# Kernel optimization log

Hardware: AMD Instinct MI355X
Metric: run time of the kernel (lower is better)

The kernel has to match this reference:

```python
import jax, jax.numpy as jnp
import numpy as np


def setup_inputs() -> dict:
    key = jax.random.key(0)
    k1, k2 = jax.random.split(key)
    B, M, N, D = 8, 2048, 2048, 1024
    x = jax.random.normal(k1, (B, M, D), dtype=jnp.float32)
    y = jax.random.normal(k2, (B, N, D), dtype=jnp.float32)
    return {"x": x, "y": y}


def reference(x, y):
    # scores e[b,m,n] = <x[b,m], y[b,n]>   (K.batch_dot(x, y, axes=2))
    e = jnp.einsum('bmd,bnd->bmn', x, y)
    # stable softmax over last axis (the exp/max/sum sequence in the original)
    p = jax.nn.softmax(e, axis=-1)
    # K.batch_dot(z, x, axes=1): contract axis 1 (m) of both -> [B, n, d]; V = x
    out = jnp.einsum('bmn,bmd->bnd', p, x)
    return out
```

## Files before the change

kernel.cpp:

```cpp
#include <hip/hip_runtime.h>
#include <hip/hip_bf16.h>
#include <stdint.h>

#define B_ 8
#define M_ 2048
#define N_ 2048
#define D_ 1024

typedef __bf16 bf16x8 __attribute__((ext_vector_type(8)));
typedef float f32x4 __attribute__((ext_vector_type(4)));
typedef uint16_t us4 __attribute__((ext_vector_type(4)));
typedef uint16_t us8 __attribute__((ext_vector_type(8)));

__device__ __forceinline__ uint16_t f2b(float f) {
    uint32_t u = __float_as_uint(f);
    return (uint16_t)((u + 0x7FFFu + ((u >> 16) & 1u)) >> 16);
}
__device__ __forceinline__ float b2f(uint16_t h) {
    return __uint_as_float(((uint32_t)h) << 16);
}

__device__ __forceinline__ void gld16(const uint16_t* g, const uint16_t* l) {
    __builtin_amdgcn_global_load_lds(
        (const __attribute__((address_space(1))) uint32_t*)g,
        (__attribute__((address_space(3))) uint32_t*)l,
        16, 0, 0);
}

__global__ __launch_bounds__(256) void k_split(const float* __restrict__ x,
                                               const float* __restrict__ y,
                                               uint16_t* __restrict__ xh, uint16_t* __restrict__ xl,
                                               uint16_t* __restrict__ yh, uint16_t* __restrict__ yl) {
    const int i = (blockIdx.x * 256 + threadIdx.x) * 4;
    float4 vx = *(const float4*)(x + i);
    float4 vy = *(const float4*)(y + i);
    float fx[4] = {vx.x, vx.y, vx.z, vx.w};
    float fy[4] = {vy.x, vy.y, vy.z, vy.w};
    us4 hx, lx, hy, ly;
#pragma unroll
    for (int k = 0; k < 4; ++k) {
        uint16_t h = f2b(fx[k]);
        hx[k] = h; lx[k] = f2b(fx[k] - b2f(h));
        uint16_t g = f2b(fy[k]);
        hy[k] = g; ly[k] = f2b(fy[k] - b2f(g));
    }
    *(us4*)(xh + i) = hx;
    *(us4*)(xl + i) = lx;
    *(us4*)(yh + i) = hy;
    *(us4*)(yl + i) = ly;
}

__global__ __launch_bounds__(256) void k_gemm1(const uint16_t* __restrict__ xh,
                                               const uint16_t* __restrict__ xl,
                                               const uint16_t* __restrict__ yh,
                                               const uint16_t* __restrict__ yl,
                                               float* __restrict__ e) {
    const int b = blockIdx.z;
    const int m0 = blockIdx.x * 128;
    const int n0 = blockIdx.y * 128;
    __shared__ __align__(16) uint16_t lds[16384];

    const int tid = threadIdx.x;
    const int lane = tid & 63;
    const int wid = tid >> 6;
    const int wm = (wid & 1) * 64;
    const int wn = (wid >> 1) * 64;
    const int quad = lane >> 4;
    const int r16 = lane & 15;
    const int swz = quad ^ ((r16 >> 1) & 3);

    const uint16_t* src[4];
    src[0] = xh + ((size_t)b * M_ + m0) * D_;
    src[1] = xl + ((size_t)b * M_ + m0) * D_;
    src[2] = yh + ((size_t)b * N_ + n0) * D_;
    src[3] = yl + ((size_t)b * N_ + n0) * D_;

    f32x4 acc[4][4];
#pragma unroll
    for (int i = 0; i < 4; ++i)
#pragma unroll
        for (int j = 0; j < 4; ++j) acc[i][j] = (f32x4){0.f, 0.f, 0.f, 0.f};

    for (int kt = 0; kt < D_ / 32; ++kt) {
#pragma unroll
        for (int c = 0; c < 8; ++c) {
            const int offbase = c * 2048 + wid * 512;
            const int tile = offbase >> 12;
            const int o = (offbase & 4095) + lane * 8;
            const int row = o >> 5;
            const int gp = (o & 31) >> 3;
            const int gd = gp ^ ((row >> 1) & 3);
            gld16(src[tile] + (size_t)row * D_ + kt * 32 + gd * 8, &lds[offbase]);
        }
        __syncthreads();

        bf16x8 ah[4], al[4], bh[4], bl[4];
#pragma unroll
        for (int i = 0; i < 4; ++i) {
            const int ra = (wm + i * 16 + r16) * 32 + swz * 8;
            ah[i] = *(const bf16x8*)&lds[ra];
            al[i] = *(const bf16x8*)&lds[4096 + ra];
            const int rb = (wn + i * 16 + r16) * 32 + swz * 8;
            bh[i] = *(const bf16x8*)&lds[8192 + rb];
            bl[i] = *(const bf16x8*)&lds[12288 + rb];
        }
#pragma unroll
        for (int i = 0; i < 4; ++i)
#pragma unroll
            for (int j = 0; j < 4; ++j) {
                acc[i][j] = __builtin_amdgcn_mfma_f32_16x16x32_bf16(ah[i], bh[j], acc[i][j], 0, 0, 0);
                acc[i][j] = __builtin_amdgcn_mfma_f32_16x16x32_bf16(ah[i], bl[j], acc[i][j], 0, 0, 0);
                acc[i][j] = __builtin_amdgcn_mfma_f32_16x16x32_bf16(al[i], bh[j], acc[i][j], 0, 0, 0);
            }
        __syncthreads();
    }

    float* eb = e + (size_t)b * M_ * N_;
#pragma unroll
    for (int i = 0; i < 4; ++i) {
        const int rbase = m0 + wm + i * 16 + quad * 4;
#pragma unroll
        for (int j = 0; j < 4; ++j) {
            const int col = n0 + wn + j * 16 + r16;
#pragma unroll
            for (int r = 0; r < 4; ++r)
                eb[(size_t)(rbase + r) * N_ + col] = acc[i][j][r];
        }
    }
}

__global__ __launch_bounds__(256) void k_rowstats(const float* __restrict__ e,
                                                  float* __restrict__ mx,
                                                  float* __restrict__ inv) {
    const int row = blockIdx.x;
    const float* p = e + (size_t)row * N_;
    const int t = threadIdx.x;
    float4 v0 = ((const float4*)p)[t];
    float4 v1 = ((const float4*)p)[t + 256];
    float m = fmaxf(fmaxf(fmaxf(v0.x, v0.y), fmaxf(v0.z, v0.w)),
                    fmaxf(fmaxf(v1.x, v1.y), fmaxf(v1.z, v1.w)));
#pragma unroll
    for (int s = 32; s > 0; s >>= 1) m = fmaxf(m, __shfl_xor(m, s, 64));
    __shared__ float smax[4];
    __shared__ float ssum[4];
    const int wid = t >> 6, lane = t & 63;
    if (lane == 0) smax[wid] = m;
    __syncthreads();
    m = fmaxf(fmaxf(smax[0], smax[1]), fmaxf(smax[2], smax[3]));
    float s = __expf(v0.x - m) + __expf(v0.y - m) + __expf(v0.z - m) + __expf(v0.w - m)
            + __expf(v1.x - m) + __expf(v1.y - m) + __expf(v1.z - m) + __expf(v1.w - m);
#pragma unroll
    for (int sh = 32; sh > 0; sh >>= 1) s += __shfl_xor(s, sh, 64);
    if (lane == 0) ssum[wid] = s;
    __syncthreads();
    if (t == 0) {
        mx[row] = m;
        inv[row] = 1.0f / (ssum[0] + ssum[1] + ssum[2] + ssum[3]);
    }
}

__global__ __launch_bounds__(256) void k_texp(const float* __restrict__ e,
                                              const float* __restrict__ mx,
                                              const float* __restrict__ inv,
                                              uint16_t* __restrict__ pT) {
    const int b = blockIdx.z, m0 = blockIdx.x * 64, n0 = blockIdx.y * 64;
    __shared__ float tile[64 * 65];
    const int t = threadIdx.x;
    const float* eb = e + (size_t)b * M_ * N_;
#pragma unroll
    for (int q = 0; q < 4; ++q) {
        const int row = q * 16 + (t >> 4);
        const int c4 = (t & 15) * 4;
        float4 v = *(const float4*)&eb[(size_t)(m0 + row) * N_ + n0 + c4];
        const float mv = mx[b * M_ + m0 + row];
        const float iv = inv[b * M_ + m0 + row];
        tile[row * 65 + c4 + 0] = __expf(v.x - mv) * iv;
        tile[row * 65 + c4 + 1] = __expf(v.y - mv) * iv;
        tile[row * 65 + c4 + 2] = __expf(v.z - mv) * iv;
        tile[row * 65 + c4 + 3] = __expf(v.w - mv) * iv;
    }
    __syncthreads();
    uint16_t* pb = pT + (size_t)b * N_ * M_;
#pragma unroll
    for (int q = 0; q < 2; ++q) {
        const int n = q * 32 + (t >> 3);
        const int mc = (t & 7) * 8;
        us8 o;
#pragma unroll
        for (int k = 0; k < 8; ++k) o[k] = f2b(tile[(mc + k) * 65 + n]);
        *(us8*)&pb[(size_t)(n0 + n) * M_ + m0 + mc] = o;
    }
}

__global__ __launch_bounds__(256) void k_tx(const float* __restrict__ x,
                                            uint16_t* __restrict__ xt) {
    const int b = blockIdx.z, m0 = blockIdx.x * 64, d0 = blockIdx.y * 64;
    __shared__ float tile[64 * 65];
    const int t = threadIdx.x;
    const float* xb = x + (size_t)b * M_ * D_;
#pragma unroll
    for (int q = 0; q < 4; ++q) {
        const int row = q * 16 + (t >> 4);
        const int c4 = (t & 15) * 4;
        float4 v = *(const float4*)&xb[(size_t)(m0 + row) * D_ + d0 + c4];
        tile[row * 65 + c4 + 0] = v.x;
        tile[row * 65 + c4 + 1] = v.y;
        tile[row * 65 + c4 + 2] = v.z;
        tile[row * 65 + c4 + 3] = v.w;
    }
    __syncthreads();
    uint16_t* xtb = xt + (size_t)b * D_ * M_;
#pragma unroll
    for (int q = 0; q < 2; ++q) {
        const int d = q * 32 + (t >> 3);
        const int mc = (t & 7) * 8;
        us8 o;
#pragma unroll
        for (int k = 0; k < 8; ++k) o[k] = f2b(tile[(mc + k) * 65 + d]);
        *(us8*)&xtb[(size_t)(d0 + d) * M_ + m0 + mc] = o;
    }
}

__global__ __launch_bounds__(256) void k_gemm2(const uint16_t* __restrict__ pT,
                                               const uint16_t* __restrict__ xt,
                                               float* __restrict__ out) {
    const int b = blockIdx.z;
    const int n0 = blockIdx.x * 128;
    const int d0 = blockIdx.y * 128;
    __shared__ __align__(16) uint16_t lds[16384];

    const int tid = threadIdx.x;
    const int lane = tid & 63;
    const int wid = tid >> 6;
    const int wn = (wid & 1) * 64;
    const int wd = (wid >> 1) * 64;
    const int quad = lane >> 4;
    const int r16 = lane & 15;

    const uint16_t* srcA = pT + ((size_t)b * N_ + n0) * M_;
    const uint16_t* srcB = xt + ((size_t)b * D_ + d0) * M_;

    f32x4 acc[4][4];
#pragma unroll
    for (int i = 0; i < 4; ++i)
#pragma unroll
        for (int j = 0; j < 4; ++j) acc[i][j] = (f32x4){0.f, 0.f, 0.f, 0.f};

    for (int kt = 0; kt < M_ / 64; ++kt) {
#pragma unroll
        for (int c = 0; c < 8; ++c) {
            const int offbase = c * 2048 + wid * 512;
            const int tile = offbase >> 13;
            const int o = (offbase & 8191) + lane * 8;
            const int row = o >> 6;
            const int gp = (o & 63) >> 3;
            const int gd = gp ^ (row & 7);
            const uint16_t* sp = tile ? srcB : srcA;
            gld16(sp + (size_t)row * M_ + kt * 64 + gd * 8, &lds[offbase]);
        }
        __syncthreads();

#pragma unroll
        for (int h = 0; h < 2; ++h) {
            const int p = (h * 4 + quad) ^ (r16 & 7);
            bf16x8 a[4], bb[4];
#pragma unroll
            for (int i = 0; i < 4; ++i) {
                a[i]  = *(const bf16x8*)&lds[(wn + i * 16 + r16) * 64 + p * 8];
                bb[i] = *(const bf16x8*)&lds[8192 + (wd + i * 16 + r16) * 64 + p * 8];
            }
#pragma unroll
            for (int i = 0; i < 4; ++i)
#pragma unroll
                for (int j = 0; j < 4; ++j)
                    acc[i][j] = __builtin_amdgcn_mfma_f32_16x16x32_bf16(a[i], bb[j], acc[i][j], 0, 0, 0);
        }
        __syncthreads();
    }

    float* ob = out + (size_t)b * N_ * D_;
#pragma unroll
    for (int i = 0; i < 4; ++i) {
        const int rbase = n0 + wn + i * 16 + quad * 4;
#pragma unroll
        for (int j = 0; j < 4; ++j) {
            const int col = d0 + wd + j * 16 + r16;
#pragma unroll
            for (int r = 0; r < 4; ++r)
                ob[(size_t)(rbase + r) * D_ + col] = acc[i][j][r];
        }
    }
}

extern "C" void kernel_launch(void* const* d_in, const int* in_sizes, int n_in,
                              void* d_out, int out_size, void* d_ws, size_t ws_size,
                              hipStream_t stream) {
    const float* x = (const float*)d_in[0];
    const float* y = (const float*)d_in[1];
    float* out = (float*)d_out;
    char* ws = (char*)d_ws;

    const size_t MiB = 1024 * 1024;
    int g = 8;
    while (g > 1 && (size_t)g * 32 * MiB > ws_size) g >>= 1;
    if ((size_t)g * 32 * MiB > ws_size) return;

    const size_t T = (size_t)g * M_ * D_ * 2;
    uint16_t* xh = (uint16_t*)(ws + 0 * T);
    uint16_t* xl = (uint16_t*)(ws + 1 * T);
    uint16_t* yh = (uint16_t*)(ws + 2 * T);
    uint16_t* yl = (uint16_t*)(ws + 3 * T);
    float*    e  = (float*)(ws + 4 * T);
    float*    mx = (float*)(ws);
    float*    inv = mx + (size_t)g * M_;
    uint16_t* xt = xl;
    uint16_t* pT = yh;

    for (int c0 = 0; c0 < B_; c0 += g) {
        const float* xc = x + (size_t)c0 * M_ * D_;
        const float* yc = y + (size_t)c0 * N_ * D_;
        float* oc = out + (size_t)c0 * N_ * D_;

        hipLaunchKernelGGL(k_split, dim3((g * M_ * D_) / (256 * 4)), dim3(256), 0, stream,
                           xc, yc, xh, xl, yh, yl);
        hipLaunchKernelGGL(k_gemm1, dim3(M_ / 128, N_ / 128, g), dim3(256), 0, stream,
                           xh, xl, yh, yl, e);
        hipLaunchKernelGGL(k_rowstats, dim3(g * M_), dim3(256), 0, stream, e, mx, inv);
        hipLaunchKernelGGL(k_texp, dim3(M_ / 64, N_ / 64, g), dim3(256), 0, stream,
                           e, mx, inv, pT);
        hipLaunchKernelGGL(k_tx, dim3(M_ / 64, D_ / 64, g), dim3(256), 0, stream, xc, xt);
        hipLaunchKernelGGL(k_gemm2, dim3(N_ / 128, D_ / 128, g), dim3(256), 0, stream,
                           pT, xt, oc);
    }
}
```

Measured before the change: 543.2 us.

## Enlarge GEMM1 tiles with double-buffered LDS and fuse partial softmax row stats

GEMM1 moves to 256x256 tiles with 512 threads, a double-buffered LDS pipeline that prefetches the next k-slice in two halves, and setprio/barrier scheduling around the MFMA groups. Its epilogue now computes per-64-column partial row max and exp-sums, and a small combine kernel merges them. This replaces the separate rowstats pass, which re-read the whole score matrix. The cost is 128 KiB of LDS per block and more registers, which limits occupancy. The partial stats are stored in the tail of the output buffer, which is safe only if that region is written after the last use.

Measured after the change: 507.4 us. -6.6%, faster.

```diff
diff --git a/kernel.cpp b/kernel.cpp
--- a/kernel.cpp
+++ b/kernel.cpp
@@ -50,113 +50,143 @@
     *(us4*)(yl + i) = ly;
 }
 
-__global__ __launch_bounds__(256) void k_gemm1(const uint16_t* __restrict__ xh,
-                                               const uint16_t* __restrict__ xl,
-                                               const uint16_t* __restrict__ yh,
-                                               const uint16_t* __restrict__ yl,
-                                               float* __restrict__ e) {
+__global__ __launch_bounds__(512, 2) void k_gemm1(const uint16_t* __restrict__ xh,
+                                                  const uint16_t* __restrict__ xl,
+                                                  const uint16_t* __restrict__ yh,
+                                                  const uint16_t* __restrict__ yl,
+                                                  float* __restrict__ e,
+                                                  float* __restrict__ pmax,
+                                                  float* __restrict__ psum) {
     const int b = blockIdx.z;
-    const int m0 = blockIdx.x * 128;
-    const int n0 = blockIdx.y * 128;
-    __shared__ __align__(16) uint16_t lds[16384];
+    const int m0 = blockIdx.x * 256;
+    const int n0 = blockIdx.y * 256;
+    __shared__ __align__(16) uint16_t lds[65536];
 
     const int tid = threadIdx.x;
     const int lane = tid & 63;
     const int wid = tid >> 6;
-    const int wm = (wid & 1) * 64;
-    const int wn = (wid >> 1) * 64;
+    const int wm = (wid >> 2) * 128;
+    const int wn = (wid & 3) * 64;
     const int quad = lane >> 4;
     const int r16 = lane & 15;
-    const int swz = quad ^ ((r16 >> 1) & 3);
-
-    const uint16_t* src[4];
-    src[0] = xh + ((size_t)b * M_ + m0) * D_;
-    src[1] = xl + ((size_t)b * M_ + m0) * D_;
-    src[2] = yh + ((size_t)b * N_ + n0) * D_;
-    src[3] = yl + ((size_t)b * N_ + n0) * D_;
-
-    f32x4 acc[4][4];
-#pragma unroll
-    for (int i = 0; i < 4; ++i)
+    const int swz8 = (quad ^ ((r16 >> 1) & 3)) * 8;
+
+    const int base_row = wid * 16 + (lane >> 2);
+    const int gd8 = ((lane & 3) ^ ((lane >> 3) & 3)) * 8;
+    const uint16_t* gp[4];
+    gp[0] = xh + ((size_t)b * M_ + m0 + base_row) * D_ + gd8;
+    gp[1] = xl + ((size_t)b * M_ + m0 + base_row) * D_ + gd8;
+    gp[2] = yh + ((size_t)b * N_ + n0 + base_row) * D_ + gd8;
+    gp[3] = yl + ((size_t)b * N_ + n0 + base_row) * D_ + gd8;
+    const int ldsW = wid * 512;
+
+    const int abase = (wm + r16) * 32 + swz8;
+    const int bbase = 16384 + (wn + r16) * 32 + swz8;
+
+    f32x4 acc[8][4];
+#pragma unroll
+    for (int i = 0; i < 8; ++i)
 #pragma unroll
         for (int j = 0; j < 4; ++j) acc[i][j] = (f32x4){0.f, 0.f, 0.f, 0.f};
 
+    auto STAGE = [&](int dst, int ktn, int c0, int c1) {
+#pragma unroll
+        for (int c = c0; c < c1; ++c)
+            gld16(gp[c >> 1] + (size_t)(c & 1) * (128 * D_) + ktn * 32,
+                  &lds[dst + c * 4096 + ldsW]);
+    };
+
+    STAGE(0, 0, 0, 8);
+
     for (int kt = 0; kt < D_ / 32; ++kt) {
-#pragma unroll
-        for (int c = 0; c < 8; ++c) {
-            const int offbase = c * 2048 + wid * 512;
-            const int tile = offbase >> 12;
-            const int o = (offbase & 4095) + lane * 8;
-            const int row = o >> 5;
-            const int gp = (o & 31) >> 3;
-            const int gd = gp ^ ((row >> 1) & 3);
-            gld16(src[tile] + (size_t)row * D_ + kt * 32 + gd * 8, &lds[offbase]);
-        }
-        __syncthreads();
-
-        bf16x8 ah[4], al[4], bh[4], bl[4];
-#pragma unroll
-        for (int i = 0; i < 4; ++i) {
-            const int ra = (wm + i * 16 + r16) * 32 + swz * 8;
-            ah[i] = *(const bf16x8*)&lds[ra];
-            al[i] = *(const bf16x8*)&lds[4096 + ra];
-            const int rb = (wn + i * 16 + r16) * 32 + swz * 8;
-            bh[i] = *(const bf16x8*)&lds[8192 + rb];
-            bl[i] = *(const bf16x8*)&lds[12288 + rb];
-        }
-#pragma unroll
-        for (int i = 0; i < 4; ++i)
+        const int bo = (kt & 1) << 15;
+        const int nbo = bo ^ 32768;
+
+        if (kt < D_ / 32 - 1) {
+            STAGE(nbo, kt + 1, 0, 4);
+            asm volatile("s_waitcnt vmcnt(4)" ::: "memory");
+        } else {
+            asm volatile("s_waitcnt vmcnt(0)" ::: "memory");
+        }
+        __builtin_amdgcn_s_barrier();
+        __builtin_amdgcn_sched_barrier(0);
+
+        bf16x8 bh[4], bl[4], ah[8], al[8];
+#pragma unroll
+        for (int j = 0; j < 4; ++j) {
+            bh[j] = *(const bf16x8*)&lds[bo + bbase + j * 512];
+            bl[j] = *(const bf16x8*)&lds[bo + bbase + 8192 + j * 512];
+        }
+        auto RDA = [&](int i) {
+            ah[i] = *(const bf16x8*)&lds[bo + abase + i * 512];
+            al[i] = *(const bf16x8*)&lds[bo + abase + 8192 + i * 512];
+        };
+        auto MM = [&](int i) {
 #pragma unroll
             for (int j = 0; j < 4; ++j) {
                 acc[i][j] = __builtin_amdgcn_mfma_f32_16x16x32_bf16(ah[i], bh[j], acc[i][j], 0, 0, 0);
                 acc[i][j] = __builtin_amdgcn_mfma_f32_16x16x32_bf16(ah[i], bl[j], acc[i][j], 0, 0, 0);
                 acc[i][j] = __builtin_amdgcn_mfma_f32_16x16x32_bf16(al[i], bh[j], acc[i][j], 0, 0, 0);
             }
-        __syncthreads();
+        };
+
+        RDA(0); RDA(1); RDA(2); RDA(3);
+        __builtin_amdgcn_s_setprio(1); MM(0); MM(1); __builtin_amdgcn_s_setprio(0);
+        __builtin_amdgcn_s_barrier(); __builtin_amdgcn_sched_barrier(0);
+        if (kt < D_ / 32 - 1) STAGE(nbo, kt + 1, 4, 8);
+        RDA(4); RDA(5);
+        __builtin_amdgcn_s_setprio(1); MM(2); MM(3); __builtin_amdgcn_s_setprio(0);
+        __builtin_amdgcn_s_barrier(); __builtin_amdgcn_sched_barrier(0);
+        RDA(6); RDA(7);
+        __builtin_amdgcn_s_setprio(1); MM(4); MM(5); __builtin_amdgcn_s_setprio(0);
+        __builtin_amdgcn_s_barrier(); __builtin_amdgcn_sched_barrier(0);
+        __builtin_amdgcn_s_setprio(1); MM(6); MM(7); __builtin_amdgcn_s_setprio(0);
+        __builtin_amdgcn_s_barrier(); __builtin_amdgcn_sched_barrier(0);
     }
 
     float* eb = e + (size_t)b * M_ * N_;
-#pragma unroll
-    for (int i = 0; i < 4; ++i) {
-        const int rbase = m0 + wm + i * 16 + quad * 4;
-#pragma unroll
-        for (int j = 0; j < 4; ++j) {
-            const int col = n0 + wn + j * 16 + r16;
-#pragma unroll
-            for (int r = 0; r < 4; ++r)
-                eb[(size_t)(rbase + r) * N_ + col] = acc[i][j][r];
-        }
-    }
-}
-
-__global__ __launch_bounds__(256) void k_rowstats(const float* __restrict__ e,
-                                                  float* __restrict__ mx,
-                                                  float* __restrict__ inv) {
-    const int row = blockIdx.x;
-    const float* p = e + (size_t)row * N_;
-    const int t = threadIdx.x;
-    float4 v0 = ((const float4*)p)[t];
-    float4 v1 = ((const float4*)p)[t + 256];
-    float m = fmaxf(fmaxf(fmaxf(v0.x, v0.y), fmaxf(v0.z, v0.w)),
-                    fmaxf(fmaxf(v1.x, v1.y), fmaxf(v1.z, v1.w)));
-#pragma unroll
-    for (int s = 32; s > 0; s >>= 1) m = fmaxf(m, __shfl_xor(m, s, 64));
-    __shared__ float smax[4];
-    __shared__ float ssum[4];
-    const int wid = t >> 6, lane = t & 63;
-    if (lane == 0) smax[wid] = m;
-    __syncthreads();
-    m = fmaxf(fmaxf(smax[0], smax[1]), fmaxf(smax[2], smax[3]));
-    float s = __expf(v0.x - m) + __expf(v0.y - m) + __expf(v0.z - m) + __expf(v0.w - m)
-            + __expf(v1.x - m) + __expf(v1.y - m) + __expf(v1.z - m) + __expf(v1.w - m);
-#pragma unroll
-    for (int sh = 32; sh > 0; sh >>= 1) s += __shfl_xor(s, sh, 64);
-    if (lane == 0) ssum[wid] = s;
-    __syncthreads();
-    if (t == 0) {
-        mx[row] = m;
-        inv[row] = 1.0f / (ssum[0] + ssum[1] + ssum[2] + ssum[3]);
-    }
+    const int grows = (int)gridDim.z * M_;
+    const int growbase = b * M_ + m0 + wm;
+    const int nb = (n0 + wn) >> 6;
+    float* pm = pmax + (size_t)nb * grows + growbase;
+    float* ps = psum + (size_t)nb * grows + growbase;
+
+#pragma unroll
+    for (int i = 0; i < 8; ++i) {
+#pragma unroll
+        for (int r = 0; r < 4; ++r) {
+            const float v0 = acc[i][0][r], v1 = acc[i][1][r];
+            const float v2 = acc[i][2][r], v3 = acc[i][3][r];
+            float mrow = fmaxf(fmaxf(v0, v1), fmaxf(v2, v3));
+#pragma unroll
+            for (int s = 1; s < 16; s <<= 1) mrow = fmaxf(mrow, __shfl_xor(mrow, s, 64));
+            float srow = __expf(v0 - mrow) + __expf(v1 - mrow)
+                       + __expf(v2 - mrow) + __expf(v3 - mrow);
+#pragma unroll
+            for (int s = 1; s < 16; s <<= 1) srow += __shfl_xor(srow, s, 64);
+            const int lrow = i * 16 + quad * 4 + r;
+            if (r16 == 0) { pm[lrow] = mrow; ps[lrow] = srow; }
+            const size_t ebase = (size_t)(m0 + wm + lrow) * N_ + n0 + wn + r16;
+#pragma unroll
+            for (int j = 0; j < 4; ++j) eb[ebase + j * 16] = acc[i][j][r];
+        }
+    }
+}
+
+__global__ __launch_bounds__(256) void k_combine(const float* __restrict__ pmax,
+                                                 const float* __restrict__ psum,
+                                                 float* __restrict__ mx,
+                                                 float* __restrict__ inv, int rows) {
+    const int r = blockIdx.x * 256 + threadIdx.x;
+    float m = -3.4e38f;
+#pragma unroll
+    for (int nb = 0; nb < 32; ++nb) m = fmaxf(m, pmax[(size_t)nb * rows + r]);
+    float s = 0.f;
+#pragma unroll
+    for (int nb = 0; nb < 32; ++nb)
+        s += psum[(size_t)nb * rows + r] * __expf(pmax[(size_t)nb * rows + r] - m);
+    mx[r] = m;
+    inv[r] = 1.0f / s;
 }
 
 __global__ __launch_bounds__(256) void k_texp(const float* __restrict__ e,
@@ -316,6 +346,10 @@
     uint16_t* xt = xl;
     uint16_t* pT = yh;
 
+    const size_t pelems = (size_t)32 * g * M_;
+    float* pmax = (float*)d_out + (size_t)B_ * N_ * D_ - 2 * pelems;
+    float* psum = pmax + pelems;
+
     for (int c0 = 0; c0 < B_; c0 += g) {
         const float* xc = x + (size_t)c0 * M_ * D_;
         const float* yc = y + (size_t)c0 * N_ * D_;
@@ -323,9 +357,10 @@
 
         hipLaunchKernelGGL(k_split, dim3((g * M_ * D_) / (256 * 4)), dim3(256), 0, stream,
                            xc, yc, xh, xl, yh, yl);
-        hipLaunchKernelGGL(k_gemm1, dim3(M_ / 128, N_ / 128, g), dim3(256), 0, stream,
-                           xh, xl, yh, yl, e);
-        hipLaunchKernelGGL(k_rowstats, dim3(g * M_), dim3(256), 0, stream, e, mx, inv);
+        hipLaunchKernelGGL(k_gemm1, dim3(M_ / 256, N_ / 256, g), dim3(512), 0, stream,
+                           xh, xl, yh, yl, e, pmax, psum);
+        hipLaunchKernelGGL(k_combine, dim3((g * M_) / 256), dim3(256), 0, stream,
+                           pmax, psum, mx, inv, g * M_);
         hipLaunchKernelGGL(k_texp, dim3(M_ / 64, N_ / 64, g), dim3(256), 0, stream,
                            e, mx, inv, pT);
         hipLaunchKernelGGL(k_tx, dim3(M_ / 64, D_ / 64, g), dim3(256), 0, stream, xc, xt);
```
